# Kernel optimization log

Hardware: AMD Instinct MI355X
Metric: run time of the kernel (lower is better)

The kernel has to match this reference:

```python
import jax, jax.numpy as jnp
import numpy as np

# Grid constants derived from init kwargs: min_pt=0, max_pt=128, step=1, eps=1e-8
ORIGIN = -(1.0 + 1e-8)          # per-dim origin of control grid
STEP = 1.0
MAX_COORD = 130.0               # control_grid_size (132) - 2
PTS_N = 2_000_000
GRID = 132
CHANNELS = 1


def setup_inputs() -> dict:
    key = jax.random.key(0)
    k1, k2 = jax.random.split(key)
    # points in world coords, uniform over the interpolable domain
    pts = jax.random.uniform(k1, (PTS_N, 3), dtype=jnp.float32) * 128.0
    control_pts = jax.random.normal(k2, (CHANNELS, GRID, GRID, GRID), dtype=jnp.float32)
    return {"pts": pts, "control_pts": control_pts}


def _coefs(x):
    # Cardinal cubic B-spline basis (Irwin-Hall n=4), x in [0,1). [pts] -> [pts,4]
    omx = 1.0 - x
    c0 = omx ** 3
    c1 = 3.0 * (x - 2.0) * x ** 2 + 4.0
    c2 = -3.0 * omx ** 2 * (x + 1.0) + 4.0
    c3 = x ** 3
    return jnp.stack([c0, c1, c2, c3], axis=-1) / 6.0


def reference(pts, control_pts):
    padding_value = 0.0
    # to control-grid coordinates
    t = (pts - ORIGIN) / STEP                                   # [P,3]
    in_bounds = jnp.all(t >= 1.0, axis=-1) & jnp.all(t < MAX_COORD, axis=-1)  # [P]
    t = jnp.where(in_bounds[:, None], t, 1.0)
    ti = t.astype(jnp.int32)                                    # trunc == floor since t>=1
    frac = t - ti.astype(t.dtype)                               # [P,3]
    w = _coefs(frac.reshape(-1)).reshape(-1, 3, 4)              # [P,3,4]

    stencil = jnp.arange(-1, 3, dtype=jnp.int32)                # [-1,0,1,2]
    idx = ti[..., None] + stencil                               # [P,3,4]
    # gather the 4x4x4 control-point stencil per point: [C,P,4,4,4]
    cp = control_pts[:, idx[:, 0, :, None, None], idx[:, 1, None, :, None], idx[:, 2, None, None, :]]
    # tensor-product weighted sum
    vals = jnp.einsum('cpijk,pi,pj,pk->pc', cp, w[:, 0], w[:, 1], w[:, 2])  # [P,C]
    vals = jnp.where(in_bounds[:, None], vals, jnp.float32(padding_value))
    return vals
```

## Files before the change

kernel.cpp:

```cpp
#include <hip/hip_runtime.h>

#define GRID_DIM 132
#define SLAB (GRID_DIM * GRID_DIM)
#define NB 512
#define CHUNK 2048
#define KPT (CHUNK / 256)
#define REG 20
#define REG3 (REG * REG * REG)
#define STRIPE 8192

__device__ __forceinline__ void bspline_w(float x, float w[4]) {
    float omx = 1.0f - x;
    w[0] = omx * omx * omx * (1.0f / 6.0f);
    w[1] = (3.0f * (x - 2.0f) * x * x + 4.0f) * (1.0f / 6.0f);
    w[2] = (-3.0f * omx * omx * (x + 1.0f) + 4.0f) * (1.0f / 6.0f);
    w[3] = x * x * x * (1.0f / 6.0f);
}

__device__ __forceinline__ void load_pt(const float* __restrict__ pts, int i,
                                        float& tx, float& ty, float& tz, bool& inb) {
    tx = pts[3 * i + 0] + 1.0f;
    ty = pts[3 * i + 1] + 1.0f;
    tz = pts[3 * i + 2] + 1.0f;
    inb = (tx >= 1.0f) && (ty >= 1.0f) && (tz >= 1.0f) &&
          (tx < 130.0f) && (ty < 130.0f) && (tz < 130.0f);
    if (!inb) { tx = ty = tz = 1.0f; }
}

__device__ __forceinline__ int calc_bin(float tx, float ty, float tz) {
    int bx = min(7, ((int)tx - 1) >> 4);
    int by = min(7, ((int)ty - 1) >> 4);
    int bz = min(7, ((int)tz - 1) >> 4);
    return (bx << 6) | (by << 3) | bz;
}

__global__ __launch_bounds__(256) void hist512_kernel(
    const float* __restrict__ pts, int n, int nblk, unsigned* __restrict__ bh)
{
    __shared__ unsigned lh[NB];
    int tid = threadIdx.x, blk = blockIdx.x;
    int c0 = blk * CHUNK;
    for (int b = tid; b < NB; b += 256) lh[b] = 0u;
    __syncthreads();
#pragma unroll
    for (int k = 0; k < KPT; ++k) {
        int i = c0 + tid + k * 256;
        if (i < n) {
            float tx, ty, tz; bool inb;
            load_pt(pts, i, tx, ty, tz, inb);
            atomicAdd(&lh[calc_bin(tx, ty, tz)], 1u);
        }
    }
    __syncthreads();
    for (int b = tid; b < NB; b += 256) bh[b * nblk + blk] = lh[b];
}

__global__ __launch_bounds__(256) void scan_l1_kernel(
    const unsigned* __restrict__ bh, unsigned* __restrict__ seg,
    unsigned* __restrict__ stot, int TOT)
{
    __shared__ unsigned sc[256];
    int t = threadIdx.x;
    int base_idx = blockIdx.x * STRIPE + t * 32;
    unsigned local[32];
    unsigned s = 0;
#pragma unroll
    for (int j = 0; j < 32; ++j) {
        int idx = base_idx + j;
        unsigned v = (idx < TOT) ? bh[idx] : 0u;
        local[j] = v; s += v;
    }
    sc[t] = s;
    __syncthreads();
    for (int off = 1; off < 256; off <<= 1) {
        unsigned v = (t >= off) ? sc[t - off] : 0u;
        __syncthreads();
        sc[t] += v;
        __syncthreads();
    }
    unsigned run = (t == 0) ? 0u : sc[t - 1];
#pragma unroll
    for (int j = 0; j < 32; ++j) {
        int idx = base_idx + j;
        if (idx < TOT) seg[idx] = run;
        run += local[j];
    }
    if (t == 255) stot[blockIdx.x] = sc[255];
}

__global__ __launch_bounds__(256) void scan_l2_kernel(
    const unsigned* __restrict__ stot, unsigned* __restrict__ soff, int nstripe)
{
    __shared__ unsigned sc[256];
    int t = threadIdx.x;
    sc[t] = (t < nstripe) ? stot[t] : 0u;
    __syncthreads();
    for (int off = 1; off < 256; off <<= 1) {
        unsigned u = (t >= off) ? sc[t - off] : 0u;
        __syncthreads();
        sc[t] += u;
        __syncthreads();
    }
    if (t < nstripe) soff[t] = (t == 0) ? 0u : sc[t - 1];
}

__global__ __launch_bounds__(256) void scan_l3_kernel(
    unsigned* __restrict__ seg, const unsigned* __restrict__ soff, int TOT)
{
    int idx = blockIdx.x * 256 + threadIdx.x;
    if (idx < TOT) seg[idx] += soff[blockIdx.x / (STRIPE / 256)];
}

__global__ __launch_bounds__(256) void partition_kernel(
    const float* __restrict__ pts, int n, int nblk,
    const unsigned* __restrict__ segstart,
    float4* __restrict__ sorted, unsigned* __restrict__ inv)
{
    __shared__ float4 buf[CHUNK];
    __shared__ unsigned lcnt[NB], lstart[NB], lcur[NB], gseg[NB];
    __shared__ unsigned sc[256];
    int tid = threadIdx.x, blk = blockIdx.x;
    int c0 = blk * CHUNK;
    int m = min(n - c0, CHUNK);

    for (int b = tid; b < NB; b += 256) lcnt[b] = 0u;
    __syncthreads();

    float4 pv[KPT];
    int bins[KPT];
#pragma unroll
    for (int k = 0; k < KPT; ++k) {
        int i = c0 + tid + k * 256;
        bins[k] = -1;
        if (i < n) {
            float tx, ty, tz; bool inb;
            load_pt(pts, i, tx, ty, tz, inb);
            unsigned tag = (unsigned)i | (inb ? 0u : 0x80000000u);
            pv[k] = make_float4(tx, ty, tz, __uint_as_float(tag));
            bins[k] = calc_bin(tx, ty, tz);
            atomicAdd(&lcnt[bins[k]], 1u);
        }
    }
    __syncthreads();

    unsigned a = lcnt[2 * tid], b2 = lcnt[2 * tid + 1];
    sc[tid] = a + b2;
    __syncthreads();
    for (int off = 1; off < 256; off <<= 1) {
        unsigned v = (tid >= off) ? sc[tid - off] : 0u;
        __syncthreads();
        sc[tid] += v;
        __syncthreads();
    }
    unsigned base = (tid == 0) ? 0u : sc[tid - 1];
    lstart[2 * tid] = base;
    lstart[2 * tid + 1] = base + a;
    __syncthreads();
    for (int b = tid; b < NB; b += 256) {
        lcur[b] = lstart[b];
        gseg[b] = segstart[b * nblk + blk];
    }
    __syncthreads();

#pragma unroll
    for (int k = 0; k < KPT; ++k) {
        if (bins[k] >= 0) {
            unsigned pos = atomicAdd(&lcur[bins[k]], 1u);
            buf[pos] = pv[k];
        }
    }
    __syncthreads();

    for (int j = tid; j < m; j += 256) {
        float4 p = buf[j];
        int b = calc_bin(p.x, p.y, p.z);
        unsigned g = gseg[b] + ((unsigned)j - lstart[b]);
        sorted[g] = p;
        inv[__float_as_uint(p.w) & 0x7fffffffu] = g;
    }
}

__global__ __launch_bounds__(256) void eval_kernel(
    const float4* __restrict__ sorted, const float* __restrict__ cp,
    const unsigned* __restrict__ segstart, float* __restrict__ val_s,
    int n, int nblk)
{
    __shared__ float region[REG3];

    int bid = blockIdx.x;
    int wg = (bid & 7) * 128 + (bid >> 3);
    int bin = wg >> 1, half = wg & 1;
    int x0 = (bin >> 6) << 4, y0 = ((bin >> 3) & 7) << 4, z0 = (bin & 7) << 4;

    const float* src = cp + (size_t)x0 * SLAB + y0 * GRID_DIM + z0;
    for (int v = threadIdx.x; v < REG3; v += 256) {
        int gx = v / (REG * REG);
        int r = v - gx * (REG * REG);
        int gy = r / REG;
        int gz = r - gy * REG;
        region[v] = src[gx * SLAB + gy * GRID_DIM + gz];
    }
    __syncthreads();

    unsigned s = segstart[bin * nblk];
    unsigned e = (bin == NB - 1) ? (unsigned)n : segstart[(bin + 1) * nblk];
    unsigned hlen = (e - s) >> 1;
    unsigned i0 = s + hlen * half;
    unsigned i1 = half ? e : s + hlen;

    for (unsigned i = i0 + threadIdx.x; i < i1; i += 256) {
        float4 p = sorted[i];
        unsigned tag = __float_as_uint(p.w);
        int ix = (int)p.x, iy = (int)p.y, iz = (int)p.z;
        float wx[4], wy[4], wz[4];
        bspline_w(p.x - (float)ix, wx);
        bspline_w(p.y - (float)iy, wy);
        bspline_w(p.z - (float)iz, wz);
        int lx = ix - 1 - x0, ly = iy - 1 - y0, lz = iz - 1 - z0;
        const float* rb = region + (lx * REG + ly) * REG + lz;
        float acc = 0.0f;
#pragma unroll
        for (int a = 0; a < 4; ++a) {
            float accy = 0.0f;
#pragma unroll
            for (int b = 0; b < 4; ++b) {
                const float* row = rb + (a * REG + b) * REG;
                float sz = fmaf(row[0], wz[0], fmaf(row[1], wz[1],
                           fmaf(row[2], wz[2], row[3] * wz[3])));
                accy = fmaf(wy[b], sz, accy);
            }
            acc = fmaf(wx[a], accy, acc);
        }
        val_s[i] = (tag >> 31) ? 0.0f : acc;
    }
}

__global__ __launch_bounds__(256) void unscatter_kernel(
    const float* __restrict__ val_s, const unsigned* __restrict__ inv,
    float* __restrict__ out, int n)
{
    int g = blockIdx.x * blockDim.x + threadIdx.x;
    int base = g * 4;
    if (base + 3 < n) {
        uint4 iv = ((const uint4*)inv)[g];
        float4 o;
        o.x = val_s[iv.x]; o.y = val_s[iv.y]; o.z = val_s[iv.z]; o.w = val_s[iv.w];
        ((float4*)out)[g] = o;
    } else if (base < n) {
        for (int k = base; k < n; ++k) out[k] = val_s[inv[k]];
    }
}

__global__ __launch_bounds__(256) void eval_unsorted_kernel(
    const float* __restrict__ pts, const float* __restrict__ cp,
    float* __restrict__ out, int n)
{
    int i = blockIdx.x * blockDim.x + threadIdx.x;
    if (i >= n) return;
    float tx, ty, tz; bool inb;
    load_pt(pts, i, tx, ty, tz, inb);
    int ix = (int)tx, iy = (int)ty, iz = (int)tz;
    float wx[4], wy[4], wz[4];
    bspline_w(tx - (float)ix, wx);
    bspline_w(ty - (float)iy, wy);
    bspline_w(tz - (float)iz, wz);
    const float* bse = cp + (size_t)(ix - 1) * SLAB + (size_t)(iy - 1) * GRID_DIM + (iz - 1);
    float acc = 0.0f;
#pragma unroll
    for (int a = 0; a < 4; ++a) {
        float accy = 0.0f;
#pragma unroll
        for (int b = 0; b < 4; ++b) {
            const float* row = bse + a * SLAB + b * GRID_DIM;
            float4 v;
            __builtin_memcpy(&v, row, 16);
            float sz = fmaf(v.x, wz[0], fmaf(v.y, wz[1], fmaf(v.z, wz[2], v.w * wz[3])));
            accy = fmaf(wy[b], sz, accy);
        }
        acc = fmaf(wx[a], accy, acc);
    }
    out[i] = inb ? acc : 0.0f;
}

extern "C" void kernel_launch(void* const* d_in, const int* in_sizes, int n_in,
                              void* d_out, int out_size, void* d_ws, size_t ws_size,
                              hipStream_t stream) {
    const float* pts = (const float*)d_in[0];
    const float* cp  = (const float*)d_in[1];
    float* out       = (float*)d_out;

    int n = in_sizes[0] / 3;
    int nblk = (n + CHUNK - 1) / CHUNK;
    int TOT = NB * nblk;
    int nstripe = (TOT + STRIPE - 1) / STRIPE;

    size_t A          = (((size_t)TOT * 4) + 1023) & ~(size_t)1023;
    size_t off_seg    = A;
    size_t off_stot   = 2 * A;
    size_t off_soff   = 2 * A + 1024;
    size_t off_sorted = 2 * A + 2048;
    size_t off_inv    = off_sorted + (size_t)n * sizeof(float4);
    size_t off_val    = off_inv    + (size_t)n * sizeof(unsigned);
    size_t need       = off_val    + (size_t)n * sizeof(float);

    if (ws_size >= need && nblk <= 1024 && nstripe <= 256) {
        unsigned* bh     = (unsigned*)d_ws;
        unsigned* seg    = (unsigned*)((char*)d_ws + off_seg);
        unsigned* stot   = (unsigned*)((char*)d_ws + off_stot);
        unsigned* soff   = (unsigned*)((char*)d_ws + off_soff);
        float4*   sorted = (float4*)((char*)d_ws + off_sorted);
        unsigned* inv    = (unsigned*)((char*)d_ws + off_inv);
        float*    val_s  = (float*)((char*)d_ws + off_val);

        int uwg = ((n + 3) / 4 + 255) / 256;

        hipLaunchKernelGGL(hist512_kernel, dim3(nblk), dim3(256), 0, stream,
                           pts, n, nblk, bh);
        hipLaunchKernelGGL(scan_l1_kernel, dim3(nstripe), dim3(256), 0, stream,
                           bh, seg, stot, TOT);
        hipLaunchKernelGGL(scan_l2_kernel, dim3(1), dim3(256), 0, stream,
                           stot, soff, nstripe);
        hipLaunchKernelGGL(scan_l3_kernel, dim3((TOT + 255) / 256), dim3(256), 0, stream,
                           seg, soff, TOT);
        hipLaunchKernelGGL(partition_kernel, dim3(nblk), dim3(256), 0, stream,
                           pts, n, nblk, seg, sorted, inv);
        hipLaunchKernelGGL(eval_kernel, dim3(1024), dim3(256), 0, stream,
                           sorted, cp, seg, val_s, n, nblk);
        hipLaunchKernelGGL(unscatter_kernel, dim3(uwg), dim3(256), 0, stream,
                           val_s, inv, out, n);
    } else {
        hipLaunchKernelGGL(eval_unsorted_kernel, dim3((n + 255) / 256), dim3(256), 0, stream,
                           pts, cp, out, n);
    }
}
```

Baseline: 167.5 us.

## Fold stripe-offset scan into consumers and drop two scan kernels

Removes the scan_l2 and scan_l3 launches. Partition and eval blocks each redo the small 256-entry stripe-offset scan in shared memory and add the offset when reading segment starts. Partition blocks are remapped so that blocks sharing an XCD handle contiguous chunks. Eval now runs one 512-thread block per bin instead of two 256-thread halves, which halves the number of region loads but reduces block count and may lower occupancy or add tail imbalance.

```diff
diff --git a/kernel.cpp b/kernel.cpp
--- a/kernel.cpp
+++ b/kernel.cpp
@@ -6,6 +6,7 @@
 #define CHUNK 2048
 #define KPT (CHUNK / 256)
 #define REG 20
+#define REG2 (REG * REG)
 #define REG3 (REG * REG * REG)
 #define STRIPE 8192
 
@@ -34,6 +35,23 @@
     return (bx << 6) | (by << 3) | bz;
 }
 
+__device__ __forceinline__ void local_stripe_scan(
+    const unsigned* __restrict__ stot, int nstripe,
+    unsigned* soff, unsigned* sc)
+{
+    int t = threadIdx.x;
+    if (t < 256) sc[t] = (t < nstripe) ? stot[t] : 0u;
+    __syncthreads();
+    for (int off = 1; off < 256; off <<= 1) {
+        unsigned v = (t >= off && t < 256) ? sc[t - off] : 0u;
+        __syncthreads();
+        if (t < 256) sc[t] += v;
+        __syncthreads();
+    }
+    if (t < 256) soff[t] = (t == 0) ? 0u : sc[t - 1];
+    __syncthreads();
+}
+
 __global__ __launch_bounds__(256) void hist512_kernel(
     const float* __restrict__ pts, int n, int nblk, unsigned* __restrict__ bh)
 {
@@ -88,38 +106,23 @@
     if (t == 255) stot[blockIdx.x] = sc[255];
 }
 
-__global__ __launch_bounds__(256) void scan_l2_kernel(
-    const unsigned* __restrict__ stot, unsigned* __restrict__ soff, int nstripe)
-{
-    __shared__ unsigned sc[256];
-    int t = threadIdx.x;
-    sc[t] = (t < nstripe) ? stot[t] : 0u;
-    __syncthreads();
-    for (int off = 1; off < 256; off <<= 1) {
-        unsigned u = (t >= off) ? sc[t - off] : 0u;
-        __syncthreads();
-        sc[t] += u;
-        __syncthreads();
-    }
-    if (t < nstripe) soff[t] = (t == 0) ? 0u : sc[t - 1];
-}
-
-__global__ __launch_bounds__(256) void scan_l3_kernel(
-    unsigned* __restrict__ seg, const unsigned* __restrict__ soff, int TOT)
-{
-    int idx = blockIdx.x * 256 + threadIdx.x;
-    if (idx < TOT) seg[idx] += soff[blockIdx.x / (STRIPE / 256)];
-}
-
 __global__ __launch_bounds__(256) void partition_kernel(
     const float* __restrict__ pts, int n, int nblk,
-    const unsigned* __restrict__ segstart,
-    float4* __restrict__ sorted, unsigned* __restrict__ inv)
+    const unsigned* __restrict__ seg, const unsigned* __restrict__ stot,
+    int nstripe, float4* __restrict__ sorted, unsigned* __restrict__ inv)
 {
     __shared__ float4 buf[CHUNK];
     __shared__ unsigned lcnt[NB], lstart[NB], lcur[NB], gseg[NB];
-    __shared__ unsigned sc[256];
-    int tid = threadIdx.x, blk = blockIdx.x;
+    __shared__ unsigned sc[256], soff[256];
+
+    local_stripe_scan(stot, nstripe, soff, sc);
+
+    int bid = blockIdx.x;
+    int q = nblk >> 3, r = nblk & 7;
+    int xcd = bid & 7, pos = bid >> 3;
+    int blk = (xcd < r ? xcd * (q + 1) : r * (q + 1) + (xcd - r) * q) + pos;
+
+    int tid = threadIdx.x;
     int c0 = blk * CHUNK;
     int m = min(n - c0, CHUNK);
 
@@ -132,7 +135,7 @@
     for (int k = 0; k < KPT; ++k) {
         int i = c0 + tid + k * 256;
         bins[k] = -1;
-        if (i < n) {
+        if (i < n && i < c0 + CHUNK) {
             float tx, ty, tz; bool inb;
             load_pt(pts, i, tx, ty, tz, inb);
             unsigned tag = (unsigned)i | (inb ? 0u : 0x80000000u);
@@ -158,15 +161,16 @@
     __syncthreads();
     for (int b = tid; b < NB; b += 256) {
         lcur[b] = lstart[b];
-        gseg[b] = segstart[b * nblk + blk];
+        int idx = b * nblk + blk;
+        gseg[b] = seg[idx] + soff[idx >> 13];
     }
     __syncthreads();
 
 #pragma unroll
     for (int k = 0; k < KPT; ++k) {
         if (bins[k] >= 0) {
-            unsigned pos = atomicAdd(&lcur[bins[k]], 1u);
-            buf[pos] = pv[k];
+            unsigned p2 = atomicAdd(&lcur[bins[k]], 1u);
+            buf[p2] = pv[k];
         }
     }
     __syncthreads();
@@ -180,35 +184,37 @@
     }
 }
 
-__global__ __launch_bounds__(256) void eval_kernel(
+__global__ __launch_bounds__(512) void eval_kernel(
     const float4* __restrict__ sorted, const float* __restrict__ cp,
-    const unsigned* __restrict__ segstart, float* __restrict__ val_s,
-    int n, int nblk)
+    const unsigned* __restrict__ seg, const unsigned* __restrict__ stot,
+    int nstripe, float* __restrict__ val_s, int n, int nblk)
 {
     __shared__ float region[REG3];
+    __shared__ unsigned sc[256], soff[256];
+
+    local_stripe_scan(stot, nstripe, soff, sc);
 
     int bid = blockIdx.x;
-    int wg = (bid & 7) * 128 + (bid >> 3);
-    int bin = wg >> 1, half = wg & 1;
+    int bin = (bid & 7) * 64 + (bid >> 3);
     int x0 = (bin >> 6) << 4, y0 = ((bin >> 3) & 7) << 4, z0 = (bin & 7) << 4;
 
     const float* src = cp + (size_t)x0 * SLAB + y0 * GRID_DIM + z0;
-    for (int v = threadIdx.x; v < REG3; v += 256) {
-        int gx = v / (REG * REG);
-        int r = v - gx * (REG * REG);
-        int gy = r / REG;
-        int gz = r - gy * REG;
+    for (int v = threadIdx.x; v < REG3; v += 512) {
+        int gx = v / REG2;
+        int rr = v - gx * REG2;
+        int gy = rr / REG;
+        int gz = rr - gy * REG;
         region[v] = src[gx * SLAB + gy * GRID_DIM + gz];
     }
     __syncthreads();
 
-    unsigned s = segstart[bin * nblk];
-    unsigned e = (bin == NB - 1) ? (unsigned)n : segstart[(bin + 1) * nblk];
-    unsigned hlen = (e - s) >> 1;
-    unsigned i0 = s + hlen * half;
-    unsigned i1 = half ? e : s + hlen;
-
-    for (unsigned i = i0 + threadIdx.x; i < i1; i += 256) {
+    int i0 = bin * nblk;
+    unsigned s = seg[i0] + soff[i0 >> 13];
+    unsigned e;
+    if (bin == NB - 1) e = (unsigned)n;
+    else { int i1 = (bin + 1) * nblk; e = seg[i1] + soff[i1 >> 13]; }
+
+    for (unsigned i = s + threadIdx.x; i < e; i += 512) {
         float4 p = sorted[i];
         unsigned tag = __float_as_uint(p.w);
         int ix = (int)p.x, iy = (int)p.y, iz = (int)p.z;
@@ -297,8 +303,7 @@
     size_t A          = (((size_t)TOT * 4) + 1023) & ~(size_t)1023;
     size_t off_seg    = A;
     size_t off_stot   = 2 * A;
-    size_t off_soff   = 2 * A + 1024;
-    size_t off_sorted = 2 * A + 2048;
+    size_t off_sorted = 2 * A + 1024;
     size_t off_inv    = off_sorted + (size_t)n * sizeof(float4);
     size_t off_val    = off_inv    + (size_t)n * sizeof(unsigned);
     size_t need       = off_val    + (size_t)n * sizeof(float);
@@ -307,7 +312,6 @@
         unsigned* bh     = (unsigned*)d_ws;
         unsigned* seg    = (unsigned*)((char*)d_ws + off_seg);
         unsigned* stot   = (unsigned*)((char*)d_ws + off_stot);
-        unsigned* soff   = (unsigned*)((char*)d_ws + off_soff);
         float4*   sorted = (float4*)((char*)d_ws + off_sorted);
         unsigned* inv    = (unsigned*)((char*)d_ws + off_inv);
         float*    val_s  = (float*)((char*)d_ws + off_val);
@@ -318,14 +322,10 @@
                            pts, n, nblk, bh);
         hipLaunchKernelGGL(scan_l1_kernel, dim3(nstripe), dim3(256), 0, stream,
                            bh, seg, stot, TOT);
-        hipLaunchKernelGGL(scan_l2_kernel, dim3(1), dim3(256), 0, stream,
-                           stot, soff, nstripe);
-        hipLaunchKernelGGL(scan_l3_kernel, dim3((TOT + 255) / 256), dim3(256), 0, stream,
-                           seg, soff, TOT);
         hipLaunchKernelGGL(partition_kernel, dim3(nblk), dim3(256), 0, stream,
-                           pts, n, nblk, seg, sorted, inv);
-        hipLaunchKernelGGL(eval_kernel, dim3(1024), dim3(256), 0, stream,
-                           sorted, cp, seg, val_s, n, nblk);
+                           pts, n, nblk, seg, stot, nstripe, sorted, inv);
+        hipLaunchKernelGGL(eval_kernel, dim3(NB), dim3(512), 0, stream,
+                           sorted, cp, seg, stot, nstripe, val_s, n, nblk);
         hipLaunchKernelGGL(unscatter_kernel, dim3(uwg), dim3(256), 0, stream,
                            val_s, inv, out, n);
     } else {
```

After: 166.2 us. No clear change (-0.8%).
